# Performance work log

Measured on AMD Instinct MI355X. Metric: run time of the kernel, lower is better.

Reference implementation:

```python
import jax, jax.numpy as jnp
import numpy as np

N_BUCKETS = 128
N_HASHES = 8
CAUSAL = True
TOKEN_SELF_ATTN_VALUE = -50000.0

B, S, D = 8, 8192, 128


def setup_inputs() -> dict:
    key = jax.random.key(0)
    k1, k2, k3 = jax.random.split(key, 3)
    vecs = jax.random.normal(k1, (B, S, D), dtype=jnp.float32)
    v = jax.random.normal(k2, (B, S, D), dtype=jnp.float32)
    rotations = jax.random.normal(k3, (1, D, N_HASHES, N_BUCKETS // 2), dtype=jnp.float32)
    return {"vecs": vecs, "v": v, "rotations": rotations}


def _look_one_back(x):
    # concat each chunk with the previous chunk (wrapping) along the intra-chunk dim
    x_extra = jnp.roll(x, 1, axis=1)
    return jnp.concatenate([x, x_extra], axis=2)


def reference(vecs, v, rotations):
    b, seqlen, dim = vecs.shape
    nh, nb = N_HASHES, N_BUCKETS

    # --- LSH hashing: random rotations + argmax over [r, -r] ---
    rot = jnp.broadcast_to(rotations, (b, dim, nh, nb // 2))
    rotated = jnp.einsum('btf,bfhi->bhti', vecs, rot)            # [b, nh, s, nb/2]
    rotated = jnp.concatenate([rotated, -rotated], axis=-1)      # [b, nh, s, nb]
    buckets = jnp.argmax(rotated, axis=-1)                       # [b, nh, s]

    offsets = (jnp.arange(nh) * nb).reshape(1, -1, 1)
    buckets = (buckets + offsets).reshape(b, nh * seqlen)        # [b, nh*s]

    ticker = jnp.broadcast_to(jnp.arange(nh * seqlen)[None, :], (b, nh * seqlen))
    buckets_and_t = seqlen * buckets + ticker % seqlen

    # sort_key_val(buckets_and_t, ticker): ticker is arange, so sticker = argsort
    sticker = jnp.argsort(buckets_and_t, axis=-1)                # [b, nh*s]
    undo_sort = jnp.argsort(sticker, axis=-1)

    st = sticker % seqlen                                        # original token positions
    sqk = jnp.take_along_axis(vecs, st[:, :, None], axis=1)      # [b, nh*s, d]
    sv = jnp.take_along_axis(v, st[:, :, None], axis=1)

    chunk_size = nh * nb
    m = (nh * seqlen) // chunk_size                              # tokens per chunk = s / nb
    bq_t = st.reshape(b, chunk_size, m)
    bqk = sqk.reshape(b, chunk_size, m, dim)
    bv = sv.reshape(b, chunk_size, m, dim)

    bq = bqk
    norm = jnp.sqrt(jnp.sum(bqk * bqk, axis=-1, keepdims=True))
    bk = bqk / jnp.maximum(norm, 1e-12)                          # F.normalize, p=2

    bk = _look_one_back(bk)                                      # [b, c, 2m, d]
    bv = _look_one_back(bv)
    bkv_t = _look_one_back(bq_t)                                 # [b, c, 2m]

    dots = jnp.einsum('bcie,bcje->bcij', bq, bk) * (dim ** -0.5) # [b, c, m, 2m]
    masked_value = -jnp.finfo(dots.dtype).max

    if CAUSAL:
        causal_mask = bq_t[:, :, :, None] < bkv_t[:, :, None, :]
        dots = jnp.where(causal_mask, masked_value, dots)

    self_mask = bq_t[:, :, :, None] == bkv_t[:, :, None, :]
    dots = jnp.where(self_mask, TOKEN_SELF_ATTN_VALUE, dots)

    return dots, undo_sort, bq_t, bkv_t, bv
```

## Files before the change

kernel.cpp:

```cpp
#include <hip/hip_runtime.h>

#define NB_B 8
#define NB_S 8192
#define NB_D 128
#define NB_H 8
#define NBUCK 128
#define NCHUNK 1024
#define CHUNK_M 64

#define OFF_DOTS 0ull
#define OFF_UNDO 67108864ull
#define OFF_BQT  67633152ull
#define OFF_BKVT 68157440ull
#define OFF_BV   69206016ull
#define BV_ELEMS 134217728ull
#define OFF_SCRATCH (OFF_BV + BV_ELEMS - 524288ull)

#define FCOMP(v, kk) ((kk) == 0 ? (v).x : (kk) == 1 ? (v).y : (kk) == 2 ? (v).z : (v).w)

typedef __attribute__((ext_vector_type(8))) short short8;
typedef __attribute__((ext_vector_type(4))) float f32x4;

static __device__ __forceinline__ unsigned short f2bf(float f) {
    unsigned u = __float_as_uint(f);
    unsigned r = (u + 0x7fffu + ((u >> 16) & 1u)) >> 16;
    return (unsigned short)r;
}

__global__ __launch_bounds__(256) void k1_buckets(
    const float* __restrict__ vecs, const float* __restrict__ rot,
    int* __restrict__ bucket)
{
    __shared__ float4 qs4[4 * 512];
    __shared__ float4 rs4[512];

    const int tid  = threadIdx.x;
    const int w    = tid >> 6;
    const int lane = tid & 63;
    const int tq   = blockIdx.x & 31;
    const int h    = (blockIdx.x >> 5) & 7;
    const int b    = blockIdx.x >> 8;
    const int tile = tq * 4 + w;

    const float4* vq    = (const float4*)vecs + ((size_t)b * NB_S + (size_t)tile * 64) * 32;
    const float*  rbase = rot + (size_t)h * 64;

    const int ig = lane >> 3;
    const int jg = lane & 7;

    float acc[8][8];
    #pragma unroll
    for (int a = 0; a < 8; ++a)
        #pragma unroll
        for (int c = 0; c < 8; ++c) acc[a][c] = 0.f;

    for (int ph = 0; ph < 4; ++ph) {
        #pragma unroll
        for (int i = 0; i < 8; ++i) {
            int idx = lane + i * 64;
            int row = idx >> 3, k4l = idx & 7;
            qs4[w * 512 + row * 8 + (k4l ^ (row & 7))] = vq[row * 32 + ph * 8 + k4l];
        }
        #pragma unroll
        for (int i = 0; i < 2; ++i) {
            int idx = tid + i * 256;
            int kl = idx >> 4, c4 = idx & 15;
            rs4[idx] = *(const float4*)(rbase + (size_t)(ph * 32 + kl) * (NB_H * 64) + c4 * 4);
        }
        __syncthreads();

        #pragma unroll
        for (int k4 = 0; k4 < 8; ++k4) {
            float4 qv[8];
            #pragma unroll
            for (int ii = 0; ii < 8; ++ii)
                qv[ii] = qs4[w * 512 + (ii * 8 + ig) * 8 + (k4 ^ ig)];
            #pragma unroll
            for (int kk = 0; kk < 4; ++kk) {
                float4 r0 = rs4[(k4 * 4 + kk) * 16 + jg * 2];
                float4 r1 = rs4[(k4 * 4 + kk) * 16 + jg * 2 + 1];
                #pragma unroll
                for (int ii = 0; ii < 8; ++ii) {
                    float q = FCOMP(qv[ii], kk);
                    acc[ii][0] = __fadd_rn(acc[ii][0], __fmul_rn(q, r0.x));
                    acc[ii][1] = __fadd_rn(acc[ii][1], __fmul_rn(q, r0.y));
                    acc[ii][2] = __fadd_rn(acc[ii][2], __fmul_rn(q, r0.z));
                    acc[ii][3] = __fadd_rn(acc[ii][3], __fmul_rn(q, r0.w));
                    acc[ii][4] = __fadd_rn(acc[ii][4], __fmul_rn(q, r1.x));
                    acc[ii][5] = __fadd_rn(acc[ii][5], __fmul_rn(q, r1.y));
                    acc[ii][6] = __fadd_rn(acc[ii][6], __fmul_rn(q, r1.z));
                    acc[ii][7] = __fadd_rn(acc[ii][7], __fmul_rn(q, r1.w));
                }
            }
        }
        __syncthreads();
    }

    float bval[8];
    int   bidx[8];
    #pragma unroll
    for (int ii = 0; ii < 8; ++ii) {
        float best = -3.4e38f;
        int   bi   = 0;
        #pragma unroll
        for (int cc = 0; cc < 8; ++cc) {
            float v = acc[ii][cc];
            if (v > best) { best = v; bi = jg * 8 + cc; }
        }
        #pragma unroll
        for (int cc = 0; cc < 8; ++cc) {
            float v = -acc[ii][cc];
            if (v > best) { best = v; bi = 64 + jg * 8 + cc; }
        }
        bval[ii] = best; bidx[ii] = bi;
    }
    #pragma unroll
    for (int off = 1; off < 8; off <<= 1) {
        #pragma unroll
        for (int ii = 0; ii < 8; ++ii) {
            float ov = __shfl_xor(bval[ii], off);
            int   oi = __shfl_xor(bidx[ii], off);
            if (ov > bval[ii] || (ov == bval[ii] && oi < bidx[ii])) {
                bval[ii] = ov; bidx[ii] = oi;
            }
        }
    }
    if (jg == 0) {
        int* bo = bucket + ((size_t)b * NB_H + h) * NB_S + (size_t)tile * 64;
        #pragma unroll
        for (int ii = 0; ii < 8; ++ii) bo[ii * 8 + ig] = bidx[ii];
    }
}

__global__ __launch_bounds__(1024) void k2_sort(
    const int* __restrict__ bucket, float* __restrict__ undo, float* __restrict__ bqt)
{
    __shared__ int   lb[NB_S];
    __shared__ short rnk[NB_S];
    __shared__ int   scnt[128 * 128];
    __shared__ int   boff[NBUCK];

    const int tid  = threadIdx.x;
    const int lane = tid & 63;
    const int wv   = tid >> 6;
    const int h = blockIdx.x & 7;
    const int b = blockIdx.x >> 3;

    const int4* src = (const int4*)(bucket + ((size_t)b * NB_H + h) * NB_S);
    #pragma unroll
    for (int i = 0; i < 2; ++i)
        ((int4*)lb)[tid + i * 1024] = src[tid + i * 1024];
    #pragma unroll
    for (int i = 0; i < 16; ++i)
        scnt[tid + i * 1024] = 0;
    __syncthreads();

    #pragma unroll
    for (int sIt = 0; sIt < 8; ++sIt) {
        int seg = wv + sIt * 16;
        int v = lb[seg * 64 + lane];
        unsigned long long same = ~0ull;
        #pragma unroll
        for (int bit = 0; bit < 7; ++bit) {
            unsigned long long m = __ballot((v >> bit) & 1);
            same &= ((v >> bit) & 1) ? m : ~m;
        }
        int rank = __popcll(same & ((1ull << lane) - 1ull));
        rnk[seg * 64 + lane] = (short)rank;
        if ((same >> lane) == 1ull)
            scnt[seg * 128 + v] = __popcll(same);
    }
    __syncthreads();

    if (tid < NBUCK) {
        int run = 0;
        for (int s = 0; s < 128; ++s) {
            int c0 = scnt[s * 128 + tid];
            scnt[s * 128 + tid] = run;
            run += c0;
        }
        boff[tid] = run;
    }
    __syncthreads();
    if (tid == 0) {
        int run = 0;
        for (int i = 0; i < NBUCK; ++i) { int c0 = boff[i]; boff[i] = run; run += c0; }
    }
    __syncthreads();

    float* bq = bqt  + (size_t)b * (NB_H * NB_S) + (size_t)h * NB_S;
    float* ud = undo + (size_t)b * (NB_H * NB_S) + (size_t)h * NB_S;
    const int pbase = h * NB_S;
    #pragma unroll
    for (int i0 = 0; i0 < 8; ++i0) {
        int i = tid + i0 * 1024;
        int v = lb[i];
        int dest = boff[v] + scnt[(i >> 6) * 128 + v] + rnk[i];
        bq[dest] = (float)i;
        ud[i]    = (float)(pbase + dest);
    }
}

#define DSTRIDE 132

__global__ __launch_bounds__(512) void k34_dots_gather(
    const float* __restrict__ vecs, const float* __restrict__ v,
    const float* __restrict__ bqt, float* __restrict__ dots,
    float* __restrict__ bkvt, float* __restrict__ bv)
{
    __shared__ union {
        short8 kds[128 * 16];
        float  dlds[64 * DSTRIDE];
    } u;
    __shared__ float  pnorm[512];
    __shared__ float  rnorm[128];
    __shared__ int    ktok[128];

    const int tid  = threadIdx.x;
    const int lane = tid & 63;
    const int w    = tid >> 6;
    const int b = blockIdx.x & 7;
    const int c = blockIdx.x >> 3;

    if (tid < 128) {
        int cc = (tid < 64) ? c : ((c + 1023) & 1023);
        int t = (int)bqt[(size_t)b * 65536 + (size_t)cc * 64 + (tid & 63)];
        ktok[tid] = t;
        bkvt[((size_t)b * NCHUNK + c) * 128 + tid] = (float)t;
    }
    __syncthreads();

    const float4* vb = (const float4*)vecs + (size_t)b * NB_S * 32;
    {
        const int row = tid >> 2, qtr = tid & 3;
        const float4* srcp = vb + (size_t)ktok[row] * 32 + qtr * 8;
        float pn = 0.f;
        #pragma unroll
        for (int j = 0; j < 4; ++j) {
            float4 x = srcp[j * 2], y = srcp[j * 2 + 1];
            pn += x.x*x.x + x.y*x.y + x.z*x.z + x.w*x.w
                + y.x*y.x + y.y*y.y + y.z*y.z + y.w*y.w;
            short8 s;
            s[0] = (short)f2bf(x.x); s[1] = (short)f2bf(x.y);
            s[2] = (short)f2bf(x.z); s[3] = (short)f2bf(x.w);
            s[4] = (short)f2bf(y.x); s[5] = (short)f2bf(y.y);
            s[6] = (short)f2bf(y.z); s[7] = (short)f2bf(y.w);
            u.kds[row * 16 + ((qtr * 4 + j) ^ (row & 7))] = s;
        }
        pnorm[tid] = pn;
    }
    __syncthreads();

    if (tid < 128)
        rnorm[tid] = 0.08838834764831845f /
            fmaxf(sqrtf(pnorm[tid * 4] + pnorm[tid * 4 + 1] +
                        pnorm[tid * 4 + 2] + pnorm[tid * 4 + 3]), 1e-12f);

    const int m  = w >> 1, nh = w & 1;
    const int cl = lane & 15;
    const int kq = lane >> 4;
    const int arow = m * 16 + cl;
    short8 a[4];
    #pragma unroll
    for (int kt = 0; kt < 4; ++kt)
        a[kt] = u.kds[arow * 16 + ((kt * 4 + kq) ^ (arow & 7))];

    f32x4 acc[4] = {};
    #pragma unroll
    for (int t = 0; t < 4; ++t) {
        const int brow = (nh * 4 + t) * 16 + cl;
        #pragma unroll
        for (int kt = 0; kt < 4; ++kt) {
            short8 bf = u.kds[brow * 16 + ((kt * 4 + kq) ^ (brow & 7))];
            acc[t] = __builtin_amdgcn_mfma_f32_16x16x32_bf16(a[kt], bf, acc[t], 0, 0, 0);
        }
    }
    __syncthreads();

    const float kMask = __uint_as_float(0xFF7F0000u);
    #pragma unroll
    for (int t = 0; t < 4; ++t) {
        const int j   = (nh * 4 + t) * 16 + cl;
        const int ktj = ktok[j];
        const float rn = rnorm[j];
        #pragma unroll
        for (int r = 0; r < 4; ++r) {
            const int i   = m * 16 + kq * 4 + r;
            const int qti = ktok[i];
            float val = acc[t][r] * rn;
            if (qti < ktj)  val = kMask;
            if (qti == ktj) val = -50000.0f;
            u.dlds[i * DSTRIDE + j] = val;
        }
    }
    __syncthreads();

    {
        float* dtile = dots + (((size_t)b * NCHUNK + c) * 64) * 128;
        #pragma unroll
        for (int i = 0; i < 4; ++i) {
            int idx = tid + i * 512;
            int row = idx >> 5, c4 = idx & 31;
            f32x4 val = *(const f32x4*)&u.dlds[row * DSTRIDE + c4 * 4];
            __builtin_nontemporal_store(val, (f32x4*)(dtile + (size_t)row * 128 + c4 * 4));
        }
    }

    const f32x4* v4 = (const f32x4*)v + (size_t)b * NB_S * 32;
    f32x4* dst = (f32x4*)bv + ((size_t)b * NCHUNK + c) * (128 * 32);
    #pragma unroll
    for (int i = 0; i < 8; ++i) {
        int idx = tid + i * 512;
        int row = idx >> 5, seg = idx & 31;
        f32x4 val = v4[(size_t)ktok[row] * 32 + seg];
        __builtin_nontemporal_store(val, &dst[idx]);
    }
}

extern "C" void kernel_launch(void* const* d_in, const int* in_sizes, int n_in,
                              void* d_out, int out_size, void* d_ws, size_t ws_size,
                              hipStream_t stream)
{
    const float* vecs = (const float*)d_in[0];
    const float* v    = (const float*)d_in[1];
    const float* rot  = (const float*)d_in[2];
    float* out = (float*)d_out;

    int* bucket = (int*)(out + OFF_SCRATCH);

    k1_buckets<<<dim3(NB_B * NB_H * (NB_S / 256)), dim3(256), 0, stream>>>(vecs, rot, bucket);
    k2_sort<<<dim3(NB_B * NB_H), dim3(1024), 0, stream>>>(bucket, out + OFF_UNDO, out + OFF_BQT);
    k34_dots_gather<<<dim3(NB_B * NCHUNK), dim3(512), 0, stream>>>(
        vecs, v, out + OFF_BQT, out + OFF_DOTS, out + OFF_BKVT, out + OFF_BV);
}
```

Measured before the change: 324.0 us.

## Compute LSH rotations one token per thread without shared-memory tiling

Rewrites the bucket-hashing kernel so each thread owns one token and accumulates all 64 rotation outputs in registers, reading the rotation matrix straight from global memory (uniform across the wave, so scalar or broadcast loads) instead of staging query and rotation tiles in LDS. This removes the LDS staging, the barriers and the cross-lane shuffle argmax reduction. In exchange, each thread reads its own strided 512-byte row with poor coalescing and holds 64 accumulators, which raises register pressure.

Result: faster. 300.2 us (-7.3%).

```diff
diff --git a/kernel.cpp b/kernel.cpp
--- a/kernel.cpp
+++ b/kernel.cpp
@@ -16,8 +16,6 @@
 #define BV_ELEMS 134217728ull
 #define OFF_SCRATCH (OFF_BV + BV_ELEMS - 524288ull)
 
-#define FCOMP(v, kk) ((kk) == 0 ? (v).x : (kk) == 1 ? (v).y : (kk) == 2 ? (v).z : (v).w)
-
 typedef __attribute__((ext_vector_type(8))) short short8;
 typedef __attribute__((ext_vector_type(4))) float f32x4;
 
@@ -31,105 +29,49 @@
     const float* __restrict__ vecs, const float* __restrict__ rot,
     int* __restrict__ bucket)
 {
-    __shared__ float4 qs4[4 * 512];
-    __shared__ float4 rs4[512];
-
     const int tid  = threadIdx.x;
     const int w    = tid >> 6;
     const int lane = tid & 63;
     const int tq   = blockIdx.x & 31;
     const int h    = (blockIdx.x >> 5) & 7;
     const int b    = blockIdx.x >> 8;
-    const int tile = tq * 4 + w;
-
-    const float4* vq    = (const float4*)vecs + ((size_t)b * NB_S + (size_t)tile * 64) * 32;
-    const float*  rbase = rot + (size_t)h * 64;
-
-    const int ig = lane >> 3;
-    const int jg = lane & 7;
-
-    float acc[8][8];
-    #pragma unroll
-    for (int a = 0; a < 8; ++a)
-        #pragma unroll
-        for (int c = 0; c < 8; ++c) acc[a][c] = 0.f;
-
-    for (int ph = 0; ph < 4; ++ph) {
-        #pragma unroll
-        for (int i = 0; i < 8; ++i) {
-            int idx = lane + i * 64;
-            int row = idx >> 3, k4l = idx & 7;
-            qs4[w * 512 + row * 8 + (k4l ^ (row & 7))] = vq[row * 32 + ph * 8 + k4l];
-        }
-        #pragma unroll
-        for (int i = 0; i < 2; ++i) {
-            int idx = tid + i * 256;
-            int kl = idx >> 4, c4 = idx & 15;
-            rs4[idx] = *(const float4*)(rbase + (size_t)(ph * 32 + kl) * (NB_H * 64) + c4 * 4);
-        }
-        __syncthreads();
-
-        #pragma unroll
-        for (int k4 = 0; k4 < 8; ++k4) {
-            float4 qv[8];
+    const int token = (tq * 4 + w) * 64 + lane;
+
+    const float* qrow  = vecs + ((size_t)b * NB_S + token) * NB_D;
+    const float* rbase = rot + (size_t)h * 64;
+
+    float acc[64];
+    #pragma unroll
+    for (int c = 0; c < 64; ++c) acc[c] = 0.f;
+
+    for (int ph = 0; ph < 16; ++ph) {
+        f32x4 q0 = *(const f32x4*)(qrow + ph * 8);
+        f32x4 q1 = *(const f32x4*)(qrow + ph * 8 + 4);
+        const float* rph = rbase + (size_t)ph * 8 * (NB_H * 64);
+        #pragma unroll
+        for (int f2 = 0; f2 < 8; ++f2) {
+            const float qf = (f2 < 4) ? q0[f2] : q1[f2 - 4];
+            const float* rrow = rph + (size_t)f2 * (NB_H * 64);
             #pragma unroll
-            for (int ii = 0; ii < 8; ++ii)
-                qv[ii] = qs4[w * 512 + (ii * 8 + ig) * 8 + (k4 ^ ig)];
-            #pragma unroll
-            for (int kk = 0; kk < 4; ++kk) {
-                float4 r0 = rs4[(k4 * 4 + kk) * 16 + jg * 2];
-                float4 r1 = rs4[(k4 * 4 + kk) * 16 + jg * 2 + 1];
-                #pragma unroll
-                for (int ii = 0; ii < 8; ++ii) {
-                    float q = FCOMP(qv[ii], kk);
-                    acc[ii][0] = __fadd_rn(acc[ii][0], __fmul_rn(q, r0.x));
-                    acc[ii][1] = __fadd_rn(acc[ii][1], __fmul_rn(q, r0.y));
-                    acc[ii][2] = __fadd_rn(acc[ii][2], __fmul_rn(q, r0.z));
-                    acc[ii][3] = __fadd_rn(acc[ii][3], __fmul_rn(q, r0.w));
-                    acc[ii][4] = __fadd_rn(acc[ii][4], __fmul_rn(q, r1.x));
-                    acc[ii][5] = __fadd_rn(acc[ii][5], __fmul_rn(q, r1.y));
-                    acc[ii][6] = __fadd_rn(acc[ii][6], __fmul_rn(q, r1.z));
-                    acc[ii][7] = __fadd_rn(acc[ii][7], __fmul_rn(q, r1.w));
-                }
-            }
-        }
-        __syncthreads();
-    }
-
-    float bval[8];
-    int   bidx[8];
-    #pragma unroll
-    for (int ii = 0; ii < 8; ++ii) {
-        float best = -3.4e38f;
-        int   bi   = 0;
-        #pragma unroll
-        for (int cc = 0; cc < 8; ++cc) {
-            float v = acc[ii][cc];
-            if (v > best) { best = v; bi = jg * 8 + cc; }
-        }
-        #pragma unroll
-        for (int cc = 0; cc < 8; ++cc) {
-            float v = -acc[ii][cc];
-            if (v > best) { best = v; bi = 64 + jg * 8 + cc; }
-        }
-        bval[ii] = best; bidx[ii] = bi;
-    }
-    #pragma unroll
-    for (int off = 1; off < 8; off <<= 1) {
-        #pragma unroll
-        for (int ii = 0; ii < 8; ++ii) {
-            float ov = __shfl_xor(bval[ii], off);
-            int   oi = __shfl_xor(bidx[ii], off);
-            if (ov > bval[ii] || (ov == bval[ii] && oi < bidx[ii])) {
-                bval[ii] = ov; bidx[ii] = oi;
-            }
-        }
-    }
-    if (jg == 0) {
-        int* bo = bucket + ((size_t)b * NB_H + h) * NB_S + (size_t)tile * 64;
-        #pragma unroll
-        for (int ii = 0; ii < 8; ++ii) bo[ii * 8 + ig] = bidx[ii];
-    }
+            for (int c = 0; c < 64; ++c)
+                acc[c] = __fadd_rn(acc[c], __fmul_rn(qf, rrow[c]));
+        }
+    }
+
+    float best = -3.4e38f;
+    int   bi   = 0;
+    #pragma unroll
+    for (int c = 0; c < 64; ++c) {
+        if (acc[c] > best) { best = acc[c]; bi = c; }
+    }
+    #pragma unroll
+    for (int c = 0; c < 64; ++c) {
+        float v = -acc[c];
+        if (v > best) { best = v; bi = 64 + c; }
+    }
+
+    int* bo = bucket + ((size_t)b * NB_H + h) * NB_S;
+    bo[token] = bi;
 }
 
 __global__ __launch_bounds__(1024) void k2_sort(
```
